# Kernel tuning notes

Hardware: AMD Instinct MI355X
Metric: run time of the kernel (lower is better)

Reference implementation:

```python
import jax, jax.numpy as jnp
import numpy as np

NQ = 4
PI_HALF = np.pi / 2
HAD = jnp.array([[1, 1], [1, -1]], dtype=jnp.complex64) / np.sqrt(2)
CNOT = jnp.array([[1, 0, 0, 0], [0, 1, 0, 0], [0, 0, 0, 1], [0, 0, 1, 0]], dtype=jnp.complex64)
_bits = (np.arange(2 ** NQ)[:, None] >> np.arange(NQ - 1, -1, -1)[None, :]) & 1
ZSIGNS = jnp.asarray(1.0 - 2.0 * _bits, jnp.float32)  # [16, NQ]


def _ry(theta):
    c = jnp.cos(theta / 2).astype(jnp.complex64)
    s = jnp.sin(theta / 2).astype(jnp.complex64)
    return jnp.stack([jnp.stack([c, -s], -1), jnp.stack([s, c], -1)], -2)  # [...,2,2]


def _rot(phi, theta, omega):
    # PennyLane Rot = RZ(omega) @ RY(theta) @ RZ(phi)
    c = jnp.cos(theta / 2).astype(jnp.complex64)
    s = jnp.sin(theta / 2).astype(jnp.complex64)
    ep = jnp.exp(0.5j * phi).astype(jnp.complex64)
    eo = jnp.exp(0.5j * omega).astype(jnp.complex64)
    return jnp.stack([jnp.stack([jnp.conj(ep) * jnp.conj(eo) * c, -ep * jnp.conj(eo) * s]),
                      jnp.stack([jnp.conj(ep) * eo * s, ep * eo * c])])


def _cry(theta):
    # controlled-RY, batched: [B] -> [B,4,4], basis order (control, target)
    B = theta.shape[0]
    U = jnp.zeros((B, 4, 4), jnp.complex64).at[:, 0, 0].set(1.0).at[:, 1, 1].set(1.0)
    return U.at[:, 2:, 2:].set(_ry(theta))


def _apply1(state, U, wire):
    s = jnp.moveaxis(state, wire + 1, 1)
    shp = s.shape
    s = s.reshape(shp[0], 2, -1)
    s = jnp.einsum('ij,bjk->bik', U, s) if U.ndim == 2 else jnp.einsum('bij,bjk->bik', U, s)
    return jnp.moveaxis(s.reshape(shp), 1, wire + 1)


def _apply2(state, U, q0, q1):
    s = jnp.moveaxis(state, (q0 + 1, q1 + 1), (1, 2))
    shp = s.shape
    s = s.reshape(shp[0], 4, -1)
    s = jnp.einsum('ij,bjk->bik', U, s) if U.ndim == 2 else jnp.einsum('bij,bjk->bik', U, s)
    return jnp.moveaxis(s.reshape(shp), (1, 2), (q0 + 1, q1 + 1))


def _init_state(B):
    s = jnp.zeros((B, 2 ** NQ), jnp.complex64).at[:, 0].set(1.0)
    return s.reshape((B,) + (2,) * NQ)


def _zexp(state):
    p = state.reshape(state.shape[0], -1)
    p = p.real ** 2 + p.imag ** 2
    return p @ ZSIGNS  # [B, NQ]


def _attention_circuit(q, k, params):
    # q, k: [E, NQ] angles; params: [NQ, 3] shared
    s = _init_state(q.shape[0])
    for i in range(NQ):
        s = _apply1(s, _ry(q[:, i]), i)
    for i in range(NQ):
        s = _apply1(s, HAD, i)
    for i in range(NQ):
        s = _apply2(s, _cry(k[:, i]), i, (i + 1) % NQ)
    for i in range(NQ):
        s = _apply1(s, _rot(params[i, 0], params[i, 1], params[i, 2]), i)
    return _zexp(s)


def _entangle_circuit(x, params):
    # x: [N, NQ] angles; params: [n_layers, NQ, 3]
    s = _init_state(x.shape[0])
    for i in range(NQ):
        s = _apply1(s, _ry(x[:, i]), i)
    for l in range(params.shape[0]):
        for i in range(NQ - 1):
            s = _apply2(s, CNOT, i, i + 1)
        for i in range(NQ):
            s = _apply1(s, _rot(params[l, i, 0], params[l, i, 1], params[l, i, 2]), i)
        s = _apply2(s, CNOT, 0, NQ - 1)  # n_qubits >= 4
    return _zexp(s)


def _path_circuit(x, params):
    # x: [N, NQ]; params: [3, NQ, 3]
    s = _init_state(x.shape[0])
    for i in range(NQ):
        s = _apply1(s, HAD, i)
    for i in range(NQ):
        s = _apply1(s, _ry(x[:, i]), i)
    for l in range(3):
        for i in range(NQ):
            s = _apply1(s, _rot(params[l, i, 0], params[l, i, 1], params[l, i, 2]), i)
        for i in range(NQ - 1):
            s = _apply2(s, CNOT, i, i + 1)
    return _zexp(s)


def _forward(x, W_in, b_in, lin_W, lin_b, qproj_W, qproj_b, ent_params,
             attq_W, attq_b, attk_W, attk_b, att_qp, path_params,
             path_in_W, path_in_b, path_out_W, path_out_b, out_W, out_b, edge_index):
    N = x.shape[0]
    loops = jnp.arange(N, dtype=edge_index.dtype)
    ei = jnp.concatenate([edge_index, jnp.stack([loops, loops])], axis=1)  # add_self_loops
    src, dst = ei[0], ei[1]
    h = jax.nn.relu(x @ W_in.T + b_in)
    for l in range(lin_W.shape[0]):
        x_cls = h @ lin_W[l].T + lin_b[l]
        xq = _entangle_circuit(jnp.tanh(h[:, :NQ]) * PI_HALF, ent_params[l])
        x_comb = x_cls + xq @ qproj_W[l].T + qproj_b[l]
        q = jnp.tanh(h @ attq_W[l].T + attq_b[l]) * PI_HALF
        k = jnp.tanh(h @ attk_W[l].T + attk_b[l]) * PI_HALF
        scores = _attention_circuit(q[src], k[dst], att_qp[l]).mean(axis=1)  # [E]
        att = jax.nn.softmax(scores)  # global softmax over all edges (faithful)
        h = jax.ops.segment_sum(att[:, None] * x_comb[src], dst, num_segments=N)
        h = jax.nn.relu(h)  # dropout is identity at eval
    pq = jnp.tanh(h @ path_in_W.T + path_in_b) * PI_HALF
    h = _path_circuit(pq, path_params) @ path_out_W.T + path_out_b
    return h @ out_W.T + out_b


def setup_inputs() -> dict:
    key = jax.random.key(0)
    ks = jax.random.split(key, 22)
    N, E, D_in, D_h, D_out, L = 20000, 300000, 64, 128, 32, 2
    w = lambda k, shape: jax.random.normal(k, shape, jnp.float32) * 0.1
    return {
        'x': jax.random.normal(ks[0], (N, D_in), jnp.float32),
        'W_in': w(ks[1], (D_h, D_in)), 'b_in': w(ks[2], (D_h,)),
        'lin_W': w(ks[3], (L, D_h, D_h)), 'lin_b': w(ks[4], (L, D_h)),
        'qproj_W': w(ks[5], (L, D_h, NQ)), 'qproj_b': w(ks[6], (L, D_h)),
        'ent_params': w(ks[7], (L, 2, NQ, 3)),
        'attq_W': w(ks[8], (L, NQ, D_h)), 'attq_b': w(ks[9], (L, NQ)),
        'attk_W': w(ks[10], (L, NQ, D_h)), 'attk_b': w(ks[11], (L, NQ)),
        'att_qp': w(ks[12], (L, NQ, 3)),
        'path_params': w(ks[13], (3, NQ, 3)),
        'path_in_W': w(ks[14], (NQ, D_h)), 'path_in_b': w(ks[15], (NQ,)),
        'path_out_W': w(ks[16], (D_h, NQ)), 'path_out_b': w(ks[17], (D_h,)),
        'out_W': w(ks[18], (D_out, D_h)), 'out_b': w(ks[19], (D_out,)),
        'edge_index': jax.random.randint(ks[20], (2, E), 0, N, dtype=jnp.int32),
    }


def reference(x, W_in, b_in, lin_W, lin_b, qproj_W, qproj_b, ent_params,
              attq_W, attq_b, attk_W, attk_b, att_qp, path_params,
              path_in_W, path_in_b, path_out_W, path_out_b, out_W, out_b, edge_index):
    return _forward(x, W_in, b_in, lin_W, lin_b, qproj_W, qproj_b, ent_params,
                    attq_W, attq_b, attk_W, attk_b, att_qp, path_params,
                    path_in_W, path_in_b, path_out_W, path_out_b, out_W, out_b, edge_index)
```

## Files before the change

kernel.cpp:

```cpp
#include <hip/hip_runtime.h>
#include <math.h>

#define PI_HALF 1.57079632679489662f

__device__ __forceinline__ float fast_tanh(float x) {
    float e = __expf(2.f * x);
    return 1.f - 2.f * __builtin_amdgcn_rcpf(e + 1.f);
}


__device__ __forceinline__ void init_state(float sr[16], float si[16]) {
#pragma unroll
    for (int i = 0; i < 16; ++i) { sr[i] = 0.f; si[i] = 0.f; }
    sr[0] = 1.f;
}

template<int M>
__device__ __forceinline__ void ry_g(float sr[16], float si[16], float c, float s) {
#pragma unroll
    for (int i = 0; i < 16; ++i) {
        if (i & M) continue;
        const int j = i | M;
        float ar = sr[i], ai = si[i], br = sr[j], bi = si[j];
        sr[i] = c * ar - s * br;  si[i] = c * ai - s * bi;
        sr[j] = s * ar + c * br;  si[j] = s * ai + c * bi;
    }
}

template<int M>
__device__ __forceinline__ void had_g(float sr[16], float si[16]) {
    const float r = 0.70710678118654752f;
#pragma unroll
    for (int i = 0; i < 16; ++i) {
        if (i & M) continue;
        const int j = i | M;
        float ar = sr[i], ai = si[i], br = sr[j], bi = si[j];
        sr[i] = (ar + br) * r;  si[i] = (ai + bi) * r;
        sr[j] = (ar - br) * r;  si[j] = (ai - bi) * r;
    }
}

template<int MC, int MT>
__device__ __forceinline__ void cnot_g(float sr[16], float si[16]) {
#pragma unroll
    for (int i = 0; i < 16; ++i) {
        if (!(i & MC) || (i & MT)) continue;
        const int j = i | MT;
        float tr = sr[i], ti = si[i];
        sr[i] = sr[j]; si[i] = si[j];
        sr[j] = tr;    si[j] = ti;
    }
}

template<int MC, int MT>
__device__ __forceinline__ void cry_g(float sr[16], float si[16], float c, float s) {
#pragma unroll
    for (int i = 0; i < 16; ++i) {
        if (!(i & MC) || (i & MT)) continue;
        const int j = i | MT;
        float ar = sr[i], ai = si[i], br = sr[j], bi = si[j];
        sr[i] = c * ar - s * br;  si[i] = c * ai - s * bi;
        sr[j] = s * ar + c * br;  si[j] = s * ai + c * bi;
    }
}

template<int M>
__device__ __forceinline__ void rot_pre(float sr[16], float si[16], const float* __restrict__ u) {
    const float u00r = u[0], u00i = u[1], u01r = u[2], u01i = u[3];
    const float u10r = u[4], u10i = u[5], u11r = u[6], u11i = u[7];
#pragma unroll
    for (int i = 0; i < 16; ++i) {
        if (i & M) continue;
        const int j = i | M;
        float ar = sr[i], ai = si[i], br = sr[j], bi = si[j];
        sr[i] = u00r * ar - u00i * ai + u01r * br - u01i * bi;
        si[i] = u00r * ai + u00i * ar + u01r * bi + u01i * br;
        sr[j] = u10r * ar - u10i * ai + u11r * br - u11i * bi;
        si[j] = u10r * ai + u10i * ar + u11r * bi + u11i * br;
    }
}

__device__ __forceinline__ void zexp_g(const float sr[16], const float si[16], float z[4]) {
    float p[16];
#pragma unroll
    for (int i = 0; i < 16; ++i) p[i] = sr[i] * sr[i] + si[i] * si[i];
    z[0] = z[1] = z[2] = z[3] = 0.f;
#pragma unroll
    for (int i = 0; i < 16; ++i) {
        z[0] += (i & 8) ? -p[i] : p[i];
        z[1] += (i & 4) ? -p[i] : p[i];
        z[2] += (i & 2) ? -p[i] : p[i];
        z[3] += (i & 1) ? -p[i] : p[i];
    }
}

__global__ void k_setup(const float* __restrict__ entp, const float* __restrict__ attqp,
                        const float* __restrict__ pparm,
                        const float* __restrict__ outW, const float* __restrict__ outb,
                        const float* __restrict__ poW, const float* __restrict__ pob,
                        float* __restrict__ rotbuf, float* __restrict__ M,
                        float* __restrict__ v) {
    const int t = threadIdx.x;
    if (t < 36) {
        const float* p;
        if (t < 16)      p = entp  + t * 3;
        else if (t < 24) p = attqp + (t - 16) * 3;
        else             p = pparm + (t - 24) * 3;
        float phi = p[0], theta = p[1], omega = p[2];
        float st, ct; sincosf(0.5f * theta, &st, &ct);
        float sp, cp; sincosf(0.5f * (phi + omega), &sp, &cp);
        float sm, cm; sincosf(0.5f * (phi - omega), &sm, &cm);
        float* u = rotbuf + t * 8;
        u[0] =  ct * cp;  u[1] = -ct * sp;
        u[2] = -st * cm;  u[3] = -st * sm;
        u[4] =  st * cm;  u[5] = -st * sm;
        u[6] =  ct * cp;  u[7] =  ct * sp;
    } else if (t >= 64 && t < 192) {
        int t2 = t - 64;
        int o = t2 >> 2, i = t2 & 3;
        float acc = 0.f;
        for (int j = 0; j < 128; ++j) acc += outW[o * 128 + j] * poW[j * 4 + i];
        M[t2] = acc;
    } else if (t >= 192 && t < 224) {
        int o = t - 192;
        float acc = outb[o];
        for (int j = 0; j < 128; ++j) acc += outW[o * 128 + j] * pob[j];
        v[o] = acc;
    }
}


__global__ void k_in(const float* __restrict__ x, const float* __restrict__ W,
                     const float* __restrict__ b, float* __restrict__ h, int N) {
    __shared__ float xs[16 * 64];
    const int base = blockIdx.x * 16;
    const int tid = threadIdx.x;
    for (int idx = tid; idx < 16 * 64; idx += 128) {
        int n = base + (idx >> 6);
        xs[idx] = (n < N) ? x[(size_t)n * 64 + (idx & 63)] : 0.f;
    }
    __syncthreads();
    float acc[16];
#pragma unroll
    for (int n = 0; n < 16; ++n) acc[n] = 0.f;
    const float4* wr4 = (const float4*)(W + tid * 64);
    for (int c4 = 0; c4 < 16; ++c4) {
        float4 w = wr4[c4];
#pragma unroll
        for (int n = 0; n < 16; ++n) {
            float4 hv = *(const float4*)&xs[n * 64 + c4 * 4];
            acc[n] += w.x * hv.x + w.y * hv.y + w.z * hv.z + w.w * hv.w;
        }
    }
    const float bb = b[tid];
#pragma unroll
    for (int n = 0; n < 16; ++n) {
        int node = base + n;
        if (node < N) h[(size_t)node * 128 + tid] = fmaxf(acc[n] + bb, 0.f);
    }
}

__global__ void k_ent(const float* __restrict__ h, const float* __restrict__ rotE,
                      float* __restrict__ xq, int N) {
    int n = blockIdx.x * blockDim.x + threadIdx.x;
    if (n >= N) return;
    float4 hv = *(const float4*)&h[(size_t)n * 128];
    float sr[16], si[16];
    init_state(sr, si);
    { float s, c; __sincosf(fast_tanh(hv.x) * (0.5f * PI_HALF), &s, &c); ry_g<8>(sr, si, c, s); }
    { float s, c; __sincosf(fast_tanh(hv.y) * (0.5f * PI_HALF), &s, &c); ry_g<4>(sr, si, c, s); }
    { float s, c; __sincosf(fast_tanh(hv.z) * (0.5f * PI_HALF), &s, &c); ry_g<2>(sr, si, c, s); }
    { float s, c; __sincosf(fast_tanh(hv.w) * (0.5f * PI_HALF), &s, &c); ry_g<1>(sr, si, c, s); }
#pragma unroll
    for (int l = 0; l < 2; ++l) {
        cnot_g<8, 4>(sr, si); cnot_g<4, 2>(sr, si); cnot_g<2, 1>(sr, si);
        const float* P = rotE + l * 32;
        rot_pre<8>(sr, si, P);
        rot_pre<4>(sr, si, P + 8);
        rot_pre<2>(sr, si, P + 16);
        rot_pre<1>(sr, si, P + 24);
        cnot_g<8, 1>(sr, si);
    }
    float z[4]; zexp_g(sr, si, z);
    *(float4*)&xq[(size_t)n * 4] = make_float4(z[0], z[1], z[2], z[3]);
}

__global__ void k_lin(const float* __restrict__ h, const float* __restrict__ xq,
                      const float* __restrict__ linW, const float* __restrict__ linb,
                      const float* __restrict__ qpW, const float* __restrict__ qpb,
                      const float* __restrict__ aqW, const float* __restrict__ aqb,
                      const float* __restrict__ akW, const float* __restrict__ akb,
                      float* __restrict__ xcomb, float* __restrict__ qbuf,
                      float* __restrict__ kbuf, int N) {
    __shared__ float hs[16 * 128];
    __shared__ float xqs[16 * 4];
    const int base = blockIdx.x * 16;
    const int tid = threadIdx.x;
    for (int idx = tid; idx < 16 * 128; idx += 128) {
        int n = base + (idx >> 7);
        hs[idx] = (n < N) ? h[(size_t)n * 128 + (idx & 127)] : 0.f;
    }
    if (tid < 64) {
        int n = base + (tid >> 2);
        xqs[tid] = (n < N) ? xq[(size_t)n * 4 + (tid & 3)] : 0.f;
    }
    __syncthreads();
    float acc[16];
#pragma unroll
    for (int n = 0; n < 16; ++n) acc[n] = 0.f;
    const float4* wr4 = (const float4*)(linW + tid * 128);
    for (int c4 = 0; c4 < 32; ++c4) {
        float4 w = wr4[c4];
#pragma unroll
        for (int n = 0; n < 16; ++n) {
            float4 hv = *(const float4*)&hs[n * 128 + c4 * 4];
            acc[n] += w.x * hv.x + w.y * hv.y + w.z * hv.z + w.w * hv.w;
        }
    }
    const float bb = linb[tid] + qpb[tid];
    const float qw0 = qpW[tid * 4 + 0], qw1 = qpW[tid * 4 + 1];
    const float qw2 = qpW[tid * 4 + 2], qw3 = qpW[tid * 4 + 3];
#pragma unroll
    for (int n = 0; n < 16; ++n) {
        int node = base + n;
        if (node < N) {
            xcomb[(size_t)node * 128 + tid] = acc[n] + bb
                + qw0 * xqs[n * 4 + 0] + qw1 * xqs[n * 4 + 1]
                + qw2 * xqs[n * 4 + 2] + qw3 * xqs[n * 4 + 3];
        }
    }
    const int nl = tid >> 3;
    const int which = tid & 7;
    const int qi = which & 3;
    const float4* Wp4 = (const float4*)(((which < 4) ? aqW : akW) + qi * 128);
    float dot = (which < 4) ? aqb[qi] : akb[qi];
    for (int c4 = 0; c4 < 32; ++c4) {
        float4 w = Wp4[c4];
        float4 hv = *(const float4*)&hs[nl * 128 + c4 * 4];
        dot += w.x * hv.x + w.y * hv.y + w.z * hv.z + w.w * hv.w;
    }
    int node = base + nl;
    if (node < N) {
        float half = fast_tanh(dot) * (0.5f * PI_HALF);
        float s, c; __sincosf(half, &s, &c);
        float* dst = ((which < 4) ? qbuf : kbuf) + (size_t)node * 8 + qi * 2;
        dst[0] = c; dst[1] = s;
    }
}

__global__ void k_att(const float* __restrict__ qb, const float* __restrict__ kb,
                      const int* __restrict__ ei, const float* __restrict__ RA,
                      const int* __restrict__ inv, float* __restrict__ escore,
                      float* __restrict__ sumexp, int E, int EP) {
    __shared__ float red[256];
    int e = blockIdx.x * blockDim.x + threadIdx.x;
    float ex = 0.f;
    if (e < EP) {
        int s_, d_;
        if (e < E) { s_ = ei[e]; d_ = ei[E + e]; } else { s_ = d_ = e - E; }
        float4 qa = *(const float4*)&qb[(size_t)s_ * 8];
        float4 qc = *(const float4*)&qb[(size_t)s_ * 8 + 4];
        float4 ka = *(const float4*)&kb[(size_t)d_ * 8];
        float4 kc = *(const float4*)&kb[(size_t)d_ * 8 + 4];
        float sr[16], si[16];
        init_state(sr, si);
        ry_g<8>(sr, si, qa.x, qa.y);
        ry_g<4>(sr, si, qa.z, qa.w);
        ry_g<2>(sr, si, qc.x, qc.y);
        ry_g<1>(sr, si, qc.z, qc.w);
        had_g<8>(sr, si); had_g<4>(sr, si); had_g<2>(sr, si); had_g<1>(sr, si);
        cry_g<8, 4>(sr, si, ka.x, ka.y);
        cry_g<4, 2>(sr, si, ka.z, ka.w);
        cry_g<2, 1>(sr, si, kc.x, kc.y);
        cry_g<1, 8>(sr, si, kc.z, kc.w);
        rot_pre<8>(sr, si, RA);
        rot_pre<4>(sr, si, RA + 8);
        rot_pre<2>(sr, si, RA + 16);
        rot_pre<1>(sr, si, RA + 24);
        float z[4]; zexp_g(sr, si, z);
        float sc = 0.25f * (z[0] + z[1] + z[2] + z[3]);
        ex = __expf(sc);
        escore[inv[e]] = ex;
    }
    red[threadIdx.x] = ex;
    __syncthreads();
    for (int s = 128; s > 0; s >>= 1) {
        if ((int)threadIdx.x < s) red[threadIdx.x] += red[threadIdx.x + s];
        __syncthreads();
    }
    if (threadIdx.x == 0) atomicAdd(sumexp, red[0]);
}


__global__ void k_hist(const int* __restrict__ ei, int* __restrict__ cnt, int E, int EP) {
    int e = blockIdx.x * blockDim.x + threadIdx.x;
    if (e >= EP) return;
    int d_ = (e < E) ? ei[E + e] : e - E;
    atomicAdd(&cnt[d_], 1);
}

__global__ void k_scan(const int* __restrict__ cnt, int* __restrict__ off,
                       int* __restrict__ cur, int N) {
    __shared__ int tot[1024];
    const int t = threadIdx.x;
    const int chunk = (N + 1023) >> 10;
    const int s0 = t * chunk;
    const int s1 = min(s0 + chunk, N);
    int sum = 0;
    for (int i = s0; i < s1; ++i) sum += cnt[i];
    tot[t] = sum;
    __syncthreads();
    for (int d = 1; d < 1024; d <<= 1) {
        int v = (t >= d) ? tot[t - d] : 0;
        __syncthreads();
        tot[t] += v;
        __syncthreads();
    }
    int run = (t == 0) ? 0 : tot[t - 1];
    for (int i = s0; i < s1; ++i) {
        off[i] = run; cur[i] = run;
        run += cnt[i];
    }
}

__global__ void k_fill(const int* __restrict__ ei, int* __restrict__ cur,
                       int* __restrict__ srcs, int* __restrict__ inv, int E, int EP) {
    int e = blockIdx.x * blockDim.x + threadIdx.x;
    if (e >= EP) return;
    int s_, d_;
    if (e < E) { s_ = ei[e]; d_ = ei[E + e]; } else { s_ = d_ = e - E; }
    int pos = atomicAdd(&cur[d_], 1);
    srcs[pos] = s_;
    inv[e] = pos;
}

__global__ void k_gather(const float* __restrict__ xcomb, const int* __restrict__ srcs,
                         const float* __restrict__ escore, const int* __restrict__ off,
                         const int* __restrict__ cnt, const float* __restrict__ sumexp,
                         float* __restrict__ h) {
    __shared__ int sS[128];
    __shared__ float wS[128];
    const int b = blockIdx.x;
    const int tid = threadIdx.x;
    const int start = off[b];
    const int num = cnt[b];
    float acc = 0.f;
    for (int base = 0; base < num; base += 128) {
        int m = min(128, num - base);
        if (tid < m) {
            sS[tid] = srcs[start + base + tid];
            wS[tid] = escore[start + base + tid];
        }
        __syncthreads();
        for (int i = 0; i < m; ++i)
            acc += wS[i] * xcomb[(size_t)sS[i] * 128 + tid];
        __syncthreads();
    }
    const float invS = __builtin_amdgcn_rcpf(sumexp[0]);
    h[(size_t)b * 128 + tid] = fmaxf(acc * invS, 0.f);
}

#define PQ_STRIDE 132
__global__ void k_pq(const float* __restrict__ h, const float* __restrict__ piW,
                     const float* __restrict__ pib, float* __restrict__ pq8, int N) {
    __shared__ float hs[32 * PQ_STRIDE];
    const int base = blockIdx.x * 32;
    const int tid = threadIdx.x;
    for (int idx = tid; idx < 32 * 128; idx += 128) {
        int n = base + (idx >> 7);
        hs[(idx >> 7) * PQ_STRIDE + (idx & 127)] = (n < N) ? h[(size_t)n * 128 + (idx & 127)] : 0.f;
    }
    __syncthreads();
    const int nl = tid >> 2;
    const int i  = tid & 3;
    float dot = pib[i];
    const float4* w4 = (const float4*)(piW + i * 128);
    for (int c4 = 0; c4 < 32; ++c4) {
        float4 w = w4[c4];
        float4 hv = *(const float4*)&hs[nl * PQ_STRIDE + c4 * 4];
        dot += w.x * hv.x + w.y * hv.y + w.z * hv.z + w.w * hv.w;
    }
    int node = base + nl;
    if (node < N) {
        float half = fast_tanh(dot) * (0.5f * PI_HALF);
        float s, c; __sincosf(half, &s, &c);
        pq8[(size_t)node * 8 + i * 2]     = c;
        pq8[(size_t)node * 8 + i * 2 + 1] = s;
    }
}

__global__ void k_pathc(const float* __restrict__ pq8, const float* __restrict__ RP,
                        const float* __restrict__ M, const float* __restrict__ v,
                        float* __restrict__ out, int N) {
    __shared__ float zS[256 * 4];
    __shared__ float MS[128];
    __shared__ float vS[32];
    const int tid = threadIdx.x;
    if (tid < 128) MS[tid] = M[tid];
    else if (tid < 160) vS[tid - 128] = v[tid - 128];
    __syncthreads();
    const int base = blockIdx.x * 256;
    const int n = base + tid;
    if (n < N) {
        float4 pa = *(const float4*)&pq8[(size_t)n * 8];
        float4 pc = *(const float4*)&pq8[(size_t)n * 8 + 4];
        float sr[16], si[16];
        init_state(sr, si);
        had_g<8>(sr, si); had_g<4>(sr, si); had_g<2>(sr, si); had_g<1>(sr, si);
        ry_g<8>(sr, si, pa.x, pa.y);
        ry_g<4>(sr, si, pa.z, pa.w);
        ry_g<2>(sr, si, pc.x, pc.y);
        ry_g<1>(sr, si, pc.z, pc.w);
#pragma unroll
        for (int l = 0; l < 3; ++l) {
            const float* P = RP + l * 32;
            rot_pre<8>(sr, si, P);
            rot_pre<4>(sr, si, P + 8);
            rot_pre<2>(sr, si, P + 16);
            rot_pre<1>(sr, si, P + 24);
            cnot_g<8, 4>(sr, si); cnot_g<4, 2>(sr, si); cnot_g<2, 1>(sr, si);
        }
        float z[4]; zexp_g(sr, si, z);
        zS[tid * 4 + 0] = z[0]; zS[tid * 4 + 1] = z[1];
        zS[tid * 4 + 2] = z[2]; zS[tid * 4 + 3] = z[3];
    }
    __syncthreads();
#pragma unroll
    for (int k = 0; k < 32; ++k) {
        int flat = k * 256 + tid;
        int nl = flat >> 5;
        int o = flat & 31;
        int node = base + nl;
        if (node < N) {
            out[(size_t)node * 32 + o] = vS[o]
                + MS[o * 4 + 0] * zS[nl * 4 + 0] + MS[o * 4 + 1] * zS[nl * 4 + 1]
                + MS[o * 4 + 2] * zS[nl * 4 + 2] + MS[o * 4 + 3] * zS[nl * 4 + 3];
        }
    }
}


extern "C" void kernel_launch(void* const* d_in, const int* in_sizes, int n_in,
                              void* d_out, int out_size, void* d_ws, size_t ws_size,
                              hipStream_t stream) {
    const float* x     = (const float*)d_in[0];
    const float* W_in  = (const float*)d_in[1];
    const float* b_in  = (const float*)d_in[2];
    const float* linW  = (const float*)d_in[3];
    const float* linb  = (const float*)d_in[4];
    const float* qpW   = (const float*)d_in[5];
    const float* qpb   = (const float*)d_in[6];
    const float* entp  = (const float*)d_in[7];
    const float* aqW   = (const float*)d_in[8];
    const float* aqb   = (const float*)d_in[9];
    const float* akW   = (const float*)d_in[10];
    const float* akb   = (const float*)d_in[11];
    const float* attqp = (const float*)d_in[12];
    const float* pparm = (const float*)d_in[13];
    const float* piW   = (const float*)d_in[14];
    const float* pib   = (const float*)d_in[15];
    const float* poW   = (const float*)d_in[16];
    const float* pob   = (const float*)d_in[17];
    const float* outW  = (const float*)d_in[18];
    const float* outb  = (const float*)d_in[19];
    const int*   ei    = (const int*)d_in[20];

    const int N  = in_sizes[0] / 64;
    const int E  = in_sizes[20] / 2;
    const int EP = E + N;

    float* ws     = (float*)d_ws;
    float* h      = ws;
    float* xcomb  = h      + (size_t)N * 128;
    float* xq     = xcomb  + (size_t)N * 128;
    float* qbuf   = xq     + (size_t)N * 4;
    float* kbuf   = qbuf   + (size_t)N * 8;
    float* pq8    = kbuf   + (size_t)N * 8;
    float* escore = pq8    + (size_t)N * 8;
    float* rotbuf = escore + EP;
    float* Mm     = rotbuf + 36 * 8;
    float* vv     = Mm + 128;
    int*   cnt    = (int*)(vv + 32);
    float* sumexp = (float*)(cnt + N);
    int*   off    = (int*)(sumexp + 4);
    int*   cur    = off + N;
    int*   srcs   = cur + N;
    int*   inv    = srcs + EP;

    const float* rotE = rotbuf;
    const float* rotA = rotbuf + 128;
    const float* rotP = rotbuf + 192;

    const int nb16 = (N + 15) / 16;
    const int ebl  = (EP + 255) / 256;

    hipMemsetAsync(cnt, 0, (size_t)(N + 4) * sizeof(int), stream);
    k_hist<<<ebl, 256, 0, stream>>>(ei, cnt, E, EP);
    k_scan<<<1, 1024, 0, stream>>>(cnt, off, cur, N);
    k_fill<<<ebl, 256, 0, stream>>>(ei, cur, srcs, inv, E, EP);
    k_setup<<<1, 256, 0, stream>>>(entp, attqp, pparm, outW, outb, poW, pob,
                                   rotbuf, Mm, vv);
    k_in<<<nb16, 128, 0, stream>>>(x, W_in, b_in, h, N);

    for (int l = 0; l < 2; ++l) {
        k_ent<<<(N + 255) / 256, 256, 0, stream>>>(h, rotE + l * 64, xq, N);
        k_lin<<<nb16, 128, 0, stream>>>(h, xq,
            linW + (size_t)l * 128 * 128, linb + l * 128,
            qpW + (size_t)l * 128 * 4, qpb + l * 128,
            aqW + (size_t)l * 4 * 128, aqb + l * 4,
            akW + (size_t)l * 4 * 128, akb + l * 4,
            xcomb, qbuf, kbuf, N);
        k_att<<<ebl, 256, 0, stream>>>(qbuf, kbuf, ei, rotA + l * 32, inv,
                                       escore, sumexp + l, E, EP);
        k_gather<<<N, 128, 0, stream>>>(xcomb, srcs, escore, off, cnt, sumexp + l, h);
    }

    k_pq<<<(N + 31) / 32, 128, 0, stream>>>(h, piW, pib, pq8, N);
    k_pathc<<<(N + 255) / 256, 256, 0, stream>>>(pq8, rotP, Mm, vv, (float*)d_out, N);
}
```

Before: 397.0 us.

## Fuse attention scoring into gather, defer softmax normalization, retile dense GEMMs

```diff
diff --git a/kernel.cpp b/kernel.cpp
--- a/kernel.cpp
+++ b/kernel.cpp
@@ -99,7 +99,7 @@
                         const float* __restrict__ outW, const float* __restrict__ outb,
                         const float* __restrict__ poW, const float* __restrict__ pob,
                         float* __restrict__ rotbuf, float* __restrict__ M,
-                        float* __restrict__ v) {
+                        float* __restrict__ v, float* __restrict__ sumexp) {
     const int t = threadIdx.x;
     if (t < 36) {
         const float* p;
@@ -126,169 +126,25 @@
         float acc = outb[o];
         for (int j = 0; j < 128; ++j) acc += outW[o * 128 + j] * pob[j];
         v[o] = acc;
-    }
-}
-
-
-__global__ void k_in(const float* __restrict__ x, const float* __restrict__ W,
-                     const float* __restrict__ b, float* __restrict__ h, int N) {
-    __shared__ float xs[16 * 64];
-    const int base = blockIdx.x * 16;
-    const int tid = threadIdx.x;
-    for (int idx = tid; idx < 16 * 64; idx += 128) {
-        int n = base + (idx >> 6);
-        xs[idx] = (n < N) ? x[(size_t)n * 64 + (idx & 63)] : 0.f;
-    }
-    __syncthreads();
-    float acc[16];
-#pragma unroll
-    for (int n = 0; n < 16; ++n) acc[n] = 0.f;
-    const float4* wr4 = (const float4*)(W + tid * 64);
-    for (int c4 = 0; c4 < 16; ++c4) {
-        float4 w = wr4[c4];
-#pragma unroll
-        for (int n = 0; n < 16; ++n) {
-            float4 hv = *(const float4*)&xs[n * 64 + c4 * 4];
-            acc[n] += w.x * hv.x + w.y * hv.y + w.z * hv.z + w.w * hv.w;
-        }
-    }
-    const float bb = b[tid];
-#pragma unroll
-    for (int n = 0; n < 16; ++n) {
-        int node = base + n;
-        if (node < N) h[(size_t)node * 128 + tid] = fmaxf(acc[n] + bb, 0.f);
-    }
-}
-
-__global__ void k_ent(const float* __restrict__ h, const float* __restrict__ rotE,
-                      float* __restrict__ xq, int N) {
-    int n = blockIdx.x * blockDim.x + threadIdx.x;
-    if (n >= N) return;
-    float4 hv = *(const float4*)&h[(size_t)n * 128];
-    float sr[16], si[16];
-    init_state(sr, si);
-    { float s, c; __sincosf(fast_tanh(hv.x) * (0.5f * PI_HALF), &s, &c); ry_g<8>(sr, si, c, s); }
-    { float s, c; __sincosf(fast_tanh(hv.y) * (0.5f * PI_HALF), &s, &c); ry_g<4>(sr, si, c, s); }
-    { float s, c; __sincosf(fast_tanh(hv.z) * (0.5f * PI_HALF), &s, &c); ry_g<2>(sr, si, c, s); }
-    { float s, c; __sincosf(fast_tanh(hv.w) * (0.5f * PI_HALF), &s, &c); ry_g<1>(sr, si, c, s); }
-#pragma unroll
-    for (int l = 0; l < 2; ++l) {
-        cnot_g<8, 4>(sr, si); cnot_g<4, 2>(sr, si); cnot_g<2, 1>(sr, si);
-        const float* P = rotE + l * 32;
-        rot_pre<8>(sr, si, P);
-        rot_pre<4>(sr, si, P + 8);
-        rot_pre<2>(sr, si, P + 16);
-        rot_pre<1>(sr, si, P + 24);
-        cnot_g<8, 1>(sr, si);
-    }
-    float z[4]; zexp_g(sr, si, z);
-    *(float4*)&xq[(size_t)n * 4] = make_float4(z[0], z[1], z[2], z[3]);
-}
-
-__global__ void k_lin(const float* __restrict__ h, const float* __restrict__ xq,
-                      const float* __restrict__ linW, const float* __restrict__ linb,
-                      const float* __restrict__ qpW, const float* __restrict__ qpb,
-                      const float* __restrict__ aqW, const float* __restrict__ aqb,
-                      const float* __restrict__ akW, const float* __restrict__ akb,
-                      float* __restrict__ xcomb, float* __restrict__ qbuf,
-                      float* __restrict__ kbuf, int N) {
-    __shared__ float hs[16 * 128];
-    __shared__ float xqs[16 * 4];
-    const int base = blockIdx.x * 16;
-    const int tid = threadIdx.x;
-    for (int idx = tid; idx < 16 * 128; idx += 128) {
-        int n = base + (idx >> 7);
-        hs[idx] = (n < N) ? h[(size_t)n * 128 + (idx & 127)] : 0.f;
-    }
-    if (tid < 64) {
-        int n = base + (tid >> 2);
-        xqs[tid] = (n < N) ? xq[(size_t)n * 4 + (tid & 3)] : 0.f;
-    }
-    __syncthreads();
-    float acc[16];
-#pragma unroll
-    for (int n = 0; n < 16; ++n) acc[n] = 0.f;
-    const float4* wr4 = (const float4*)(linW + tid * 128);
-    for (int c4 = 0; c4 < 32; ++c4) {
-        float4 w = wr4[c4];
-#pragma unroll
-        for (int n = 0; n < 16; ++n) {
-            float4 hv = *(const float4*)&hs[n * 128 + c4 * 4];
-            acc[n] += w.x * hv.x + w.y * hv.y + w.z * hv.z + w.w * hv.w;
-        }
-    }
-    const float bb = linb[tid] + qpb[tid];
-    const float qw0 = qpW[tid * 4 + 0], qw1 = qpW[tid * 4 + 1];
-    const float qw2 = qpW[tid * 4 + 2], qw3 = qpW[tid * 4 + 3];
-#pragma unroll
-    for (int n = 0; n < 16; ++n) {
-        int node = base + n;
-        if (node < N) {
-            xcomb[(size_t)node * 128 + tid] = acc[n] + bb
-                + qw0 * xqs[n * 4 + 0] + qw1 * xqs[n * 4 + 1]
-                + qw2 * xqs[n * 4 + 2] + qw3 * xqs[n * 4 + 3];
-        }
-    }
-    const int nl = tid >> 3;
-    const int which = tid & 7;
-    const int qi = which & 3;
-    const float4* Wp4 = (const float4*)(((which < 4) ? aqW : akW) + qi * 128);
-    float dot = (which < 4) ? aqb[qi] : akb[qi];
-    for (int c4 = 0; c4 < 32; ++c4) {
-        float4 w = Wp4[c4];
-        float4 hv = *(const float4*)&hs[nl * 128 + c4 * 4];
-        dot += w.x * hv.x + w.y * hv.y + w.z * hv.z + w.w * hv.w;
-    }
-    int node = base + nl;
-    if (node < N) {
-        float half = fast_tanh(dot) * (0.5f * PI_HALF);
-        float s, c; __sincosf(half, &s, &c);
-        float* dst = ((which < 4) ? qbuf : kbuf) + (size_t)node * 8 + qi * 2;
-        dst[0] = c; dst[1] = s;
-    }
-}
-
-__global__ void k_att(const float* __restrict__ qb, const float* __restrict__ kb,
-                      const int* __restrict__ ei, const float* __restrict__ RA,
-                      const int* __restrict__ inv, float* __restrict__ escore,
-                      float* __restrict__ sumexp, int E, int EP) {
-    __shared__ float red[256];
-    int e = blockIdx.x * blockDim.x + threadIdx.x;
-    float ex = 0.f;
-    if (e < EP) {
-        int s_, d_;
-        if (e < E) { s_ = ei[e]; d_ = ei[E + e]; } else { s_ = d_ = e - E; }
-        float4 qa = *(const float4*)&qb[(size_t)s_ * 8];
-        float4 qc = *(const float4*)&qb[(size_t)s_ * 8 + 4];
-        float4 ka = *(const float4*)&kb[(size_t)d_ * 8];
-        float4 kc = *(const float4*)&kb[(size_t)d_ * 8 + 4];
-        float sr[16], si[16];
-        init_state(sr, si);
-        ry_g<8>(sr, si, qa.x, qa.y);
-        ry_g<4>(sr, si, qa.z, qa.w);
-        ry_g<2>(sr, si, qc.x, qc.y);
-        ry_g<1>(sr, si, qc.z, qc.w);
-        had_g<8>(sr, si); had_g<4>(sr, si); had_g<2>(sr, si); had_g<1>(sr, si);
-        cry_g<8, 4>(sr, si, ka.x, ka.y);
-        cry_g<4, 2>(sr, si, ka.z, ka.w);
-        cry_g<2, 1>(sr, si, kc.x, kc.y);
-        cry_g<1, 8>(sr, si, kc.z, kc.w);
-        rot_pre<8>(sr, si, RA);
-        rot_pre<4>(sr, si, RA + 8);
-        rot_pre<2>(sr, si, RA + 16);
-        rot_pre<1>(sr, si, RA + 24);
-        float z[4]; zexp_g(sr, si, z);
-        float sc = 0.25f * (z[0] + z[1] + z[2] + z[3]);
-        ex = __expf(sc);
-        escore[inv[e]] = ex;
-    }
-    red[threadIdx.x] = ex;
-    __syncthreads();
-    for (int s = 128; s > 0; s >>= 1) {
-        if ((int)threadIdx.x < s) red[threadIdx.x] += red[threadIdx.x + s];
-        __syncthreads();
-    }
-    if (threadIdx.x == 0) atomicAdd(sumexp, red[0]);
+    } else if (t == 255) {
+        sumexp[0] = 1.0f;
+    }
+}
+
+__global__ void k_tr(const float* __restrict__ Win, const float* __restrict__ l0,
+                     const float* __restrict__ l1, float* __restrict__ tWin,
+                     float* __restrict__ tl0, float* __restrict__ tl1) {
+    int i = blockIdx.x * 256 + threadIdx.x;
+    if (i < 64 * 128) {
+        int k = i >> 7, o = i & 127;
+        tWin[i] = Win[o * 64 + k];
+    }
+    int j = i - 64 * 128;
+    if (j >= 0 && j < 128 * 128) {
+        int k = j >> 7, o = j & 127;
+        tl0[j] = l0[o * 128 + k];
+        tl1[j] = l1[o * 128 + k];
+    }
 }
 
 
@@ -324,51 +180,265 @@
 }
 
 __global__ void k_fill(const int* __restrict__ ei, int* __restrict__ cur,
-                       int* __restrict__ srcs, int* __restrict__ inv, int E, int EP) {
+                       int* __restrict__ srcs, int E, int EP) {
     int e = blockIdx.x * blockDim.x + threadIdx.x;
     if (e >= EP) return;
     int s_, d_;
     if (e < E) { s_ = ei[e]; d_ = ei[E + e]; } else { s_ = d_ = e - E; }
     int pos = atomicAdd(&cur[d_], 1);
     srcs[pos] = s_;
-    inv[e] = pos;
-}
-
-__global__ void k_gather(const float* __restrict__ xcomb, const int* __restrict__ srcs,
-                         const float* __restrict__ escore, const int* __restrict__ off,
-                         const int* __restrict__ cnt, const float* __restrict__ sumexp,
-                         float* __restrict__ h) {
+}
+
+
+#define XS 68
+__global__ __launch_bounds__(256) void k_in(
+        const float* __restrict__ x, const float* __restrict__ tW,
+        const float* __restrict__ b, float* __restrict__ h, int N) {
+    __shared__ float xs[64 * XS];
+    const int base = blockIdx.x * 64;
+    const int tid = threadIdx.x;
+    for (int idx = tid; idx < 64 * 64; idx += 256) {
+        int n = base + (idx >> 6);
+        xs[(idx >> 6) * XS + (idx & 63)] = (n < N) ? x[(size_t)n * 64 + (idx & 63)] : 0.f;
+    }
+    __syncthreads();
+    const int og = tid & 15;
+    const int ng = tid >> 4;
+    float acc[8][4];
+#pragma unroll
+    for (int r = 0; r < 8; ++r)
+#pragma unroll
+        for (int n = 0; n < 4; ++n) acc[r][n] = 0.f;
+    for (int k4 = 0; k4 < 16; ++k4) {
+        float4 hv[4];
+#pragma unroll
+        for (int n = 0; n < 4; ++n) hv[n] = *(const float4*)&xs[(ng * 4 + n) * XS + k4 * 4];
+#pragma unroll
+        for (int j = 0; j < 4; ++j) {
+            const float* wr = tW + (k4 * 4 + j) * 128 + og * 8;
+            float4 w0 = *(const float4*)wr;
+            float4 w1 = *(const float4*)(wr + 4);
+#pragma unroll
+            for (int n = 0; n < 4; ++n) {
+                float hj = (&hv[n].x)[j];
+                acc[0][n] += w0.x * hj; acc[1][n] += w0.y * hj;
+                acc[2][n] += w0.z * hj; acc[3][n] += w0.w * hj;
+                acc[4][n] += w1.x * hj; acc[5][n] += w1.y * hj;
+                acc[6][n] += w1.z * hj; acc[7][n] += w1.w * hj;
+            }
+        }
+    }
+    float4 b0 = *(const float4*)&b[og * 8];
+    float4 b1 = *(const float4*)&b[og * 8 + 4];
+#pragma unroll
+    for (int n = 0; n < 4; ++n) {
+        int node = base + ng * 4 + n;
+        if (node < N) {
+            float4 o0 = make_float4(fmaxf(acc[0][n] + b0.x, 0.f), fmaxf(acc[1][n] + b0.y, 0.f),
+                                    fmaxf(acc[2][n] + b0.z, 0.f), fmaxf(acc[3][n] + b0.w, 0.f));
+            float4 o1 = make_float4(fmaxf(acc[4][n] + b1.x, 0.f), fmaxf(acc[5][n] + b1.y, 0.f),
+                                    fmaxf(acc[6][n] + b1.z, 0.f), fmaxf(acc[7][n] + b1.w, 0.f));
+            *(float4*)&h[(size_t)node * 128 + og * 8] = o0;
+            *(float4*)&h[(size_t)node * 128 + og * 8 + 4] = o1;
+        }
+    }
+}
+
+__global__ void k_ent(const float* __restrict__ h, const float* __restrict__ rotE,
+                      const float* __restrict__ pS, float* __restrict__ xq, int N) {
+    int n = blockIdx.x * blockDim.x + threadIdx.x;
+    if (n >= N) return;
+    const float invS = __builtin_amdgcn_rcpf(pS[0]);
+    float4 hv = *(const float4*)&h[(size_t)n * 128];
+    float sr[16], si[16];
+    init_state(sr, si);
+    { float s, c; __sincosf(fast_tanh(hv.x * invS) * (0.5f * PI_HALF), &s, &c); ry_g<8>(sr, si, c, s); }
+    { float s, c; __sincosf(fast_tanh(hv.y * invS) * (0.5f * PI_HALF), &s, &c); ry_g<4>(sr, si, c, s); }
+    { float s, c; __sincosf(fast_tanh(hv.z * invS) * (0.5f * PI_HALF), &s, &c); ry_g<2>(sr, si, c, s); }
+    { float s, c; __sincosf(fast_tanh(hv.w * invS) * (0.5f * PI_HALF), &s, &c); ry_g<1>(sr, si, c, s); }
+#pragma unroll
+    for (int l = 0; l < 2; ++l) {
+        cnot_g<8, 4>(sr, si); cnot_g<4, 2>(sr, si); cnot_g<2, 1>(sr, si);
+        const float* P = rotE + l * 32;
+        rot_pre<8>(sr, si, P);
+        rot_pre<4>(sr, si, P + 8);
+        rot_pre<2>(sr, si, P + 16);
+        rot_pre<1>(sr, si, P + 24);
+        cnot_g<8, 1>(sr, si);
+    }
+    float z[4]; zexp_g(sr, si, z);
+    *(float4*)&xq[(size_t)n * 4] = make_float4(z[0], z[1], z[2], z[3]);
+}
+
+#define HS 132
+__global__ __launch_bounds__(256) void k_lin(
+        const float* __restrict__ h, const float* __restrict__ xq,
+        const float* __restrict__ tlinW, const float* __restrict__ linb,
+        const float* __restrict__ qpW, const float* __restrict__ qpb,
+        const float* __restrict__ aqW, const float* __restrict__ aqb,
+        const float* __restrict__ akW, const float* __restrict__ akb,
+        const float* __restrict__ pS,
+        float* __restrict__ xcomb, float* __restrict__ qbuf,
+        float* __restrict__ kbuf, int N) {
+    __shared__ float hs[64 * HS];
+    __shared__ float zS[64 * 4];
+    const int base = blockIdx.x * 64;
+    const int tid = threadIdx.x;
+    const float invS = __builtin_amdgcn_rcpf(pS[0]);
+    for (int idx = tid; idx < 64 * 128; idx += 256) {
+        int n = base + (idx >> 7);
+        hs[(idx >> 7) * HS + (idx & 127)] =
+            (n < N) ? h[(size_t)n * 128 + (idx & 127)] * invS : 0.f;
+    }
+    {
+        int n = base + (tid >> 2);
+        zS[tid] = (n < N) ? xq[(size_t)n * 4 + (tid & 3)] : 0.f;
+    }
+    __syncthreads();
+
+    const int og = tid & 15;
+    const int ng = tid >> 4;
+    float acc[8][4];
+#pragma unroll
+    for (int r = 0; r < 8; ++r)
+#pragma unroll
+        for (int n = 0; n < 4; ++n) acc[r][n] = 0.f;
+    for (int k4 = 0; k4 < 32; ++k4) {
+        float4 hv[4];
+#pragma unroll
+        for (int n = 0; n < 4; ++n) hv[n] = *(const float4*)&hs[(ng * 4 + n) * HS + k4 * 4];
+#pragma unroll
+        for (int j = 0; j < 4; ++j) {
+            const float* wr = tlinW + (k4 * 4 + j) * 128 + og * 8;
+            float4 w0 = *(const float4*)wr;
+            float4 w1 = *(const float4*)(wr + 4);
+#pragma unroll
+            for (int n = 0; n < 4; ++n) {
+                float hj = (&hv[n].x)[j];
+                acc[0][n] += w0.x * hj; acc[1][n] += w0.y * hj;
+                acc[2][n] += w0.z * hj; acc[3][n] += w0.w * hj;
+                acc[4][n] += w1.x * hj; acc[5][n] += w1.y * hj;
+                acc[6][n] += w1.z * hj; acc[7][n] += w1.w * hj;
+            }
+        }
+    }
+
+    {
+        const int nl = tid >> 2;
+        const int qi = tid & 3;
+        const float4* Wq4 = (const float4*)(aqW + qi * 128);
+        const float4* Wk4 = (const float4*)(akW + qi * 128);
+        float dq = aqb[qi], dk = akb[qi];
+        for (int c4 = 0; c4 < 32; ++c4) {
+            float4 hv = *(const float4*)&hs[nl * HS + c4 * 4];
+            float4 wq = Wq4[c4], wk = Wk4[c4];
+            dq += wq.x * hv.x + wq.y * hv.y + wq.z * hv.z + wq.w * hv.w;
+            dk += wk.x * hv.x + wk.y * hv.y + wk.z * hv.z + wk.w * hv.w;
+        }
+        int node = base + nl;
+        if (node < N) {
+            float s, c;
+            __sincosf(fast_tanh(dq) * (0.5f * PI_HALF), &s, &c);
+            qbuf[(size_t)node * 8 + qi * 2] = c;
+            qbuf[(size_t)node * 8 + qi * 2 + 1] = s;
+            __sincosf(fast_tanh(dk) * (0.5f * PI_HALF), &s, &c);
+            kbuf[(size_t)node * 8 + qi * 2] = c;
+            kbuf[(size_t)node * 8 + qi * 2 + 1] = s;
+        }
+    }
+
+    const float4 lb0 = *(const float4*)&linb[og * 8];
+    const float4 lb1 = *(const float4*)&linb[og * 8 + 4];
+    const float4 qb0 = *(const float4*)&qpb[og * 8];
+    const float4 qb1 = *(const float4*)&qpb[og * 8 + 4];
+#pragma unroll
+    for (int n = 0; n < 4; ++n) {
+        int node = base + ng * 4 + n;
+        if (node < N) {
+            float4 z = *(const float4*)&zS[(ng * 4 + n) * 4];
+            float4 o0, o1;
+            const float* qw = qpW + og * 32;
+            o0.x = acc[0][n] + lb0.x + qb0.x + qw[0]*z.x + qw[1]*z.y + qw[2]*z.z + qw[3]*z.w;
+            o0.y = acc[1][n] + lb0.y + qb0.y + qw[4]*z.x + qw[5]*z.y + qw[6]*z.z + qw[7]*z.w;
+            o0.z = acc[2][n] + lb0.z + qb0.z + qw[8]*z.x + qw[9]*z.y + qw[10]*z.z + qw[11]*z.w;
+            o0.w = acc[3][n] + lb0.w + qb0.w + qw[12]*z.x + qw[13]*z.y + qw[14]*z.z + qw[15]*z.w;
+            o1.x = acc[4][n] + lb1.x + qb1.x + qw[16]*z.x + qw[17]*z.y + qw[18]*z.z + qw[19]*z.w;
+            o1.y = acc[5][n] + lb1.y + qb1.y + qw[20]*z.x + qw[21]*z.y + qw[22]*z.z + qw[23]*z.w;
+            o1.z = acc[6][n] + lb1.z + qb1.z + qw[24]*z.x + qw[25]*z.y + qw[26]*z.z + qw[27]*z.w;
+            o1.w = acc[7][n] + lb1.w + qb1.w + qw[28]*z.x + qw[29]*z.y + qw[30]*z.z + qw[31]*z.w;
+            *(float4*)&xcomb[(size_t)node * 128 + og * 8] = o0;
+            *(float4*)&xcomb[(size_t)node * 128 + og * 8 + 4] = o1;
+        }
+    }
+}
+
+__global__ __launch_bounds__(128) void k_gatt(
+        const float* __restrict__ qb, const float* __restrict__ kb,
+        const int* __restrict__ srcs, const int* __restrict__ off,
+        const int* __restrict__ cnt, const float* __restrict__ xcomb,
+        const float* __restrict__ RA, float* __restrict__ g,
+        float* __restrict__ sumexp_next, int N) {
     __shared__ int sS[128];
     __shared__ float wS[128];
+    __shared__ float red[2];
     const int b = blockIdx.x;
     const int tid = threadIdx.x;
     const int start = off[b];
     const int num = cnt[b];
-    float acc = 0.f;
-    for (int base = 0; base < num; base += 128) {
-        int m = min(128, num - base);
+    float4 ka = *(const float4*)&kb[(size_t)b * 8];
+    float4 kc = *(const float4*)&kb[(size_t)b * 8 + 4];
+    float acc = 0.f, exsum = 0.f;
+    for (int base2 = 0; base2 < num; base2 += 128) {
+        int m = min(128, num - base2);
         if (tid < m) {
-            sS[tid] = srcs[start + base + tid];
-            wS[tid] = escore[start + base + tid];
+            int s_ = srcs[start + base2 + tid];
+            float4 qa = *(const float4*)&qb[(size_t)s_ * 8];
+            float4 qc = *(const float4*)&qb[(size_t)s_ * 8 + 4];
+            float sr[16], si[16];
+            init_state(sr, si);
+            ry_g<8>(sr, si, qa.x, qa.y);
+            ry_g<4>(sr, si, qa.z, qa.w);
+            ry_g<2>(sr, si, qc.x, qc.y);
+            ry_g<1>(sr, si, qc.z, qc.w);
+            had_g<8>(sr, si); had_g<4>(sr, si); had_g<2>(sr, si); had_g<1>(sr, si);
+            cry_g<8, 4>(sr, si, ka.x, ka.y);
+            cry_g<4, 2>(sr, si, ka.z, ka.w);
+            cry_g<2, 1>(sr, si, kc.x, kc.y);
+            cry_g<1, 8>(sr, si, kc.z, kc.w);
+            rot_pre<8>(sr, si, RA);
+            rot_pre<4>(sr, si, RA + 8);
+            rot_pre<2>(sr, si, RA + 16);
+            rot_pre<1>(sr, si, RA + 24);
+            float z[4]; zexp_g(sr, si, z);
+            float sc = 0.25f * (z[0] + z[1] + z[2] + z[3]);
+            float ex = __expf(sc);
+            sS[tid] = s_; wS[tid] = ex;
+            exsum += ex;
         }
         __syncthreads();
         for (int i = 0; i < m; ++i)
             acc += wS[i] * xcomb[(size_t)sS[i] * 128 + tid];
         __syncthreads();
     }
-    const float invS = __builtin_amdgcn_rcpf(sumexp[0]);
-    h[(size_t)b * 128 + tid] = fmaxf(acc * invS, 0.f);
-}
-
-#define PQ_STRIDE 132
+    g[(size_t)b * 128 + tid] = fmaxf(acc, 0.f);
+#pragma unroll
+    for (int d = 32; d > 0; d >>= 1) exsum += __shfl_down(exsum, d, 64);
+    if ((tid & 63) == 0) red[tid >> 6] = exsum;
+    __syncthreads();
+    if (tid == 0) atomicAdd(sumexp_next, red[0] + red[1]);
+}
+
 __global__ void k_pq(const float* __restrict__ h, const float* __restrict__ piW,
-                     const float* __restrict__ pib, float* __restrict__ pq8, int N) {
-    __shared__ float hs[32 * PQ_STRIDE];
+                     const float* __restrict__ pib, const float* __restrict__ pS,
+                     float* __restrict__ pq8, int N) {
+    __shared__ float hs[32 * HS];
     const int base = blockIdx.x * 32;
     const int tid = threadIdx.x;
+    const float invS = __builtin_amdgcn_rcpf(pS[0]);
     for (int idx = tid; idx < 32 * 128; idx += 128) {
         int n = base + (idx >> 7);
-        hs[(idx >> 7) * PQ_STRIDE + (idx & 127)] = (n < N) ? h[(size_t)n * 128 + (idx & 127)] : 0.f;
+        hs[(idx >> 7) * HS + (idx & 127)] =
+            (n < N) ? h[(size_t)n * 128 + (idx & 127)] * invS : 0.f;
     }
     __syncthreads();
     const int nl = tid >> 2;
@@ -377,13 +447,12 @@
     const float4* w4 = (const float4*)(piW + i * 128);
     for (int c4 = 0; c4 < 32; ++c4) {
         float4 w = w4[c4];
-        float4 hv = *(const float4*)&hs[nl * PQ_STRIDE + c4 * 4];
+        float4 hv = *(const float4*)&hs[nl * HS + c4 * 4];
         dot += w.x * hv.x + w.y * hv.y + w.z * hv.z + w.w * hv.w;
     }
     int node = base + nl;
     if (node < N) {
-        float half = fast_tanh(dot) * (0.5f * PI_HALF);
-        float s, c; __sincosf(half, &s, &c);
+        float s, c; __sincosf(fast_tanh(dot) * (0.5f * PI_HALF), &s, &c);
         pq8[(size_t)node * 8 + i * 2]     = c;
         pq8[(size_t)node * 8 + i * 2 + 1] = s;
     }
@@ -476,8 +545,10 @@
     float* qbuf   = xq     + (size_t)N * 4;
     float* kbuf   = qbuf   + (size_t)N * 8;
     float* pq8    = kbuf   + (size_t)N * 8;
-    float* escore = pq8    + (size_t)N * 8;
-    float* rotbuf = escore + EP;
+    float* tWin   = pq8    + (size_t)N * 8;
+    float* tl0    = tWin   + 64 * 128;
+    float* tl1    = tl0    + 128 * 128;
+    float* rotbuf = tl1    + 128 * 128;
     float* Mm     = rotbuf + 36 * 8;
     float* vv     = Mm + 128;
     int*   cnt    = (int*)(vv + 32);
@@ -485,36 +556,36 @@
     int*   off    = (int*)(sumexp + 4);
     int*   cur    = off + N;
     int*   srcs   = cur + N;
-    int*   inv    = srcs + EP;
 
     const float* rotE = rotbuf;
     const float* rotA = rotbuf + 128;
     const float* rotP = rotbuf + 192;
 
-    const int nb16 = (N + 15) / 16;
+    const int nb64 = (N + 63) / 64;
     const int ebl  = (EP + 255) / 256;
 
     hipMemsetAsync(cnt, 0, (size_t)(N + 4) * sizeof(int), stream);
     k_hist<<<ebl, 256, 0, stream>>>(ei, cnt, E, EP);
     k_scan<<<1, 1024, 0, stream>>>(cnt, off, cur, N);
-    k_fill<<<ebl, 256, 0, stream>>>(ei, cur, srcs, inv, E, EP);
+    k_fill<<<ebl, 256, 0, stream>>>(ei, cur, srcs, E, EP);
     k_setup<<<1, 256, 0, stream>>>(entp, attqp, pparm, outW, outb, poW, pob,
-                                   rotbuf, Mm, vv);
-    k_in<<<nb16, 128, 0, stream>>>(x, W_in, b_in, h, N);
+                                   rotbuf, Mm, vv, sumexp);
+    k_tr<<<96, 256, 0, stream>>>(W_in, linW, linW + 128 * 128, tWin, tl0, tl1);
+    k_in<<<nb64, 256, 0, stream>>>(x, tWin, b_in, h, N);
 
     for (int l = 0; l < 2; ++l) {
-        k_ent<<<(N + 255) / 256, 256, 0, stream>>>(h, rotE + l * 64, xq, N);
-        k_lin<<<nb16, 128, 0, stream>>>(h, xq,
-            linW + (size_t)l * 128 * 128, linb + l * 128,
+        const float* tl = (l == 0) ? tl0 : tl1;
+        k_ent<<<(N + 255) / 256, 256, 0, stream>>>(h, rotE + l * 64, sumexp + l, xq, N);
+        k_lin<<<nb64, 256, 0, stream>>>(h, xq, tl,
+            linb + l * 128,
             qpW + (size_t)l * 128 * 4, qpb + l * 128,
             aqW + (size_t)l * 4 * 128, aqb + l * 4,
             akW + (size_t)l * 4 * 128, akb + l * 4,
-            xcomb, qbuf, kbuf, N);
-        k_att<<<ebl, 256, 0, stream>>>(qbuf, kbuf, ei, rotA + l * 32, inv,
-                                       escore, sumexp + l, E, EP);
-        k_gather<<<N, 128, 0, stream>>>(xcomb, srcs, escore, off, cnt, sumexp + l, h);
-    }
-
-    k_pq<<<(N + 31) / 32, 128, 0, stream>>>(h, piW, pib, pq8, N);
+            sumexp + l, xcomb, qbuf, kbuf, N);
+        k_gatt<<<N, 128, 0, stream>>>(qbuf, kbuf, srcs, off, cnt, xcomb,
+                                      rotA + l * 32, h, sumexp + l + 1, N);
+    }
+
+    k_pq<<<(N + 31) / 32, 128, 0, stream>>>(h, piW, pib, sumexp + 2, pq8, N);
     k_pathc<<<(N + 255) / 256, 256, 0, stream>>>(pq8, rotP, Mm, vv, (float*)d_out, N);
 }
```

Measured after the change: 850.6 us. 114% more time.
